# Performance work log

Measured on AMD Instinct MI355X. Metric: run time of the kernel, lower is better.

## Reference

```python
import jax, jax.numpy as jnp
import numpy as np

HEADS = 16


def setup_inputs() -> dict:
    key = jax.random.key(0)
    ks = jax.random.split(key, 7)
    b, n, dim = 4, 1024, 1024
    s = 1.0 / np.sqrt(dim)
    return {
        "x": jax.random.normal(ks[0], (b, n, dim), dtype=jnp.float32),
        "Wq": jax.random.normal(ks[1], (dim, dim), dtype=jnp.float32) * s,
        "bq": jax.random.normal(ks[2], (dim,), dtype=jnp.float32) * 0.01,
        "Wv": jax.random.normal(ks[3], (dim, dim), dtype=jnp.float32) * s,
        "bv": jax.random.normal(ks[4], (dim,), dtype=jnp.float32) * 0.01,
        "Wo": jax.random.normal(ks[5], (dim, dim), dtype=jnp.float32) * s,
        "bo": jax.random.normal(ks[6], (dim,), dtype=jnp.float32) * 0.01,
    }


def reference(x, Wq, bq, Wv, bv, Wo, bo):
    b, n, dim = x.shape
    h = HEADS
    d = dim // h
    scale = d ** -0.5

    # projections (torch Linear: x @ W.T + b), split heads: b n (h d) -> b h n d
    q = (x @ Wq.T + bq).reshape(b, n, h, d).transpose(0, 2, 1, 3)
    v = (x @ Wv.T + bv).reshape(b, n, h, d).transpose(0, 2, 1, 3)

    # pairwise L2 distance scores: ||q_i||^2 - 2 q_i.q_j + ||q_j||^2
    dots = jnp.einsum("bhnd,bhmd->bhnm", q, q)          # [b,h,n,n]
    sq = jnp.sum(q * q, axis=-1)                          # [b,h,n]
    scores = -(sq[..., :, None] - 2.0 * dots + sq[..., None, :]) * scale
    attn = jax.nn.softmax(scores, axis=-1)

    out = jnp.einsum("bhnm,bhmd->bhnd", attn, v)          # [b,h,n,d]
    out = out.transpose(0, 2, 1, 3).reshape(b, n, dim)    # b h n d -> b n (h d)
    return out @ Wo.T + bo
```

## Files before the change

kernel.cpp:

```cpp
#include <hip/hip_runtime.h>
#include <hip/hip_bf16.h>

typedef __hip_bfloat16 bf16;
typedef short short8 __attribute__((ext_vector_type(8)));
typedef float floatx4 __attribute__((ext_vector_type(4)));
typedef unsigned uintx4 __attribute__((ext_vector_type(4)));
typedef unsigned short ushort;

#define MFMA __builtin_amdgcn_mfma_f32_16x16x32_bf16

#define BATCH 4
#define SEQ   1024
#define DIM   1024
#define HEADS 16
#define HD    64
#define RS    72


__device__ __forceinline__ float b2f(ushort u) {
    union { unsigned i; float f; } x; x.i = (unsigned)u << 16; return x.f;
}
__device__ __forceinline__ ushort f2b(float f) {
    union { float f; unsigned i; } x; x.f = f;
    return (ushort)((x.i + 0x7FFFu + ((x.i >> 16) & 1u)) >> 16);
}

__device__ __forceinline__ void nts16(void* p, uint4 v) {
    uintx4 x; x.x = v.x; x.y = v.y; x.z = v.z; x.w = v.w;
    __builtin_nontemporal_store(x, (uintx4*)p);
}
__device__ __forceinline__ void nts16f(void* p, float4 v) {
    floatx4 x; x.x = v.x; x.y = v.y; x.z = v.z; x.w = v.w;
    __builtin_nontemporal_store(x, (floatx4*)p);
}
__device__ __forceinline__ void nts2(ushort* p, ushort v) {
    __builtin_nontemporal_store(v, p);
}

__device__ __forceinline__ void gload16(const ushort* gp, ushort* lp) {
    __builtin_amdgcn_global_load_lds(
        (const __attribute__((address_space(1))) unsigned*)gp,
        (__attribute__((address_space(3))) unsigned*)lp, 16, 0, 0);
}

__device__ __forceinline__ short8 cvt8(uint4 a, uint4 b) {
    const float* f0 = (const float*)&a;
    const float* f1 = (const float*)&b;
    union { __hip_bfloat162 h; unsigned u; } c0, c1, c2, c3;
    float2 p;
    p.x = f0[0]; p.y = f0[1]; c0.h = __float22bfloat162_rn(p);
    p.x = f0[2]; p.y = f0[3]; c1.h = __float22bfloat162_rn(p);
    p.x = f1[0]; p.y = f1[1]; c2.h = __float22bfloat162_rn(p);
    p.x = f1[2]; p.y = f1[3]; c3.h = __float22bfloat162_rn(p);
    short8 s;
    unsigned* su = (unsigned*)&s;
    su[0] = c0.u; su[1] = c1.u; su[2] = c2.u; su[3] = c3.u;
    return s;
}

__global__ __launch_bounds__(256)
void conv_all(const float* __restrict__ x,  const float* __restrict__ Wq,
              const float* __restrict__ Wv, const float* __restrict__ Wo,
              ushort* __restrict__ xb,  ushort* __restrict__ wqb,
              ushort* __restrict__ wvb, ushort* __restrict__ wob, int doWo)
{
    const int b = blockIdx.x;
    const float* src; ushort* dst; size_t off;
    if (b < 2048)      { src = x;  dst = xb;  off = (size_t)b * 256; }
    else if (b < 2560) { src = Wq; dst = wqb; off = (size_t)(b - 2048) * 256; }
    else if (b < 3072) { src = Wv; dst = wvb; off = (size_t)(b - 2560) * 256; }
    else               { if (!doWo) return;
                         src = Wo; dst = wob; off = (size_t)(b - 3072) * 256; }
    off += threadIdx.x;
    const uint4* sv = (const uint4*)src;
    uint4 a = sv[off * 2], c = sv[off * 2 + 1];
    short8 s = cvt8(a, c);
    nts16(dst + off * 8, *(uint4*)&s);
}

template<int OUT, int BDMA>
__global__ __launch_bounds__(256, 3)
void gemm_core(const ushort* __restrict__ Ab,
               const ushort* __restrict__ Wb0, const ushort* __restrict__ Wb1,
               const float* __restrict__ Wf,
               const float* __restrict__ b0, const float* __restrict__ b1,
               ushort* __restrict__ Qd, ushort* __restrict__ Vd,
               float* __restrict__ Fd, float* __restrict__ sqQ)
{
    __shared__ __align__(16) ushort SMEM[2 * 8192 + 2 * 64 * RS];
    const int t = threadIdx.x;
    const int w = t >> 6, lane = t & 63;
    const int lr = lane & 15, quad = lane >> 4;
    const int isV = (!OUT) && (blockIdx.x >= 16);
    const int n0 = (blockIdx.x & 15) * 64;
    const int m0 = blockIdx.y * 128;
    const ushort* __restrict__ Wb   = isV ? Wb1 : Wb0;
    const float*  __restrict__ bias = isV ? b1 : b0;
    const int mw = (w >> 1) * 64, nw = (w & 1) * 32;
    const int ar = t >> 3, ac8 = (t & 7) * 8;
    const int arow = lane >> 3;
    const int acS  = ((lane & 7) ^ arow) * 8;

    ushort* Acur = SMEM;
    ushort* Anxt = SMEM + 8192;
    ushort* Bcur = SMEM + 16384;
    ushort* Bnxt = SMEM + 16384 + (BDMA ? 4096 : 64 * RS);

    uint4 wpre[4];
    #pragma unroll
    for (int i = 0; i < 4; ++i) {
        const int chunk = w * 4 + i;
        gload16(Ab + (size_t)(m0 + chunk * 8 + arow) * DIM + acS,
                Acur + chunk * 512);
    }
    if (BDMA) {
        #pragma unroll
        for (int i = 0; i < 2; ++i) {
            const int c = w * 2 + i;
            gload16(Wb + (size_t)(n0 + c * 8 + arow) * DIM + acS,
                    Bcur + c * 512);
        }
    } else {
        #pragma unroll
        for (int c = 0; c < 2; ++c) {
            const float* wp = Wf + (size_t)(n0 + c * 32 + ar) * DIM + ac8;
            wpre[2 * c]     = *(const uint4*)wp;
            wpre[2 * c + 1] = *(const uint4*)(wp + 4);
        }
        #pragma unroll
        for (int c = 0; c < 2; ++c)
            *(short8*)&Bcur[(c * 32 + ar) * RS + ac8] = cvt8(wpre[2 * c], wpre[2 * c + 1]);
    }
    __syncthreads();

    floatx4 acc[4][2];
    const floatx4 fz = {0.f, 0.f, 0.f, 0.f};
    #pragma unroll
    for (int i = 0; i < 4; ++i)
        #pragma unroll
        for (int j = 0; j < 2; ++j) acc[i][j] = fz;

    for (int kt = 0; kt < 16; ++kt) {
        if (kt < 15) {
            const int k0 = (kt + 1) * 64;
            #pragma unroll
            for (int i = 0; i < 4; ++i) {
                const int chunk = w * 4 + i;
                gload16(Ab + (size_t)(m0 + chunk * 8 + arow) * DIM + k0 + acS,
                        Anxt + chunk * 512);
            }
            if (BDMA) {
                #pragma unroll
                for (int i = 0; i < 2; ++i) {
                    const int c = w * 2 + i;
                    gload16(Wb + (size_t)(n0 + c * 8 + arow) * DIM + k0 + acS,
                            Bnxt + c * 512);
                }
            } else {
                #pragma unroll
                for (int c = 0; c < 2; ++c) {
                    const float* wp = Wf + (size_t)(n0 + c * 32 + ar) * DIM + k0 + ac8;
                    wpre[2 * c]     = *(const uint4*)wp;
                    wpre[2 * c + 1] = *(const uint4*)(wp + 4);
                }
            }
        }
        #pragma unroll
        for (int ks = 0; ks < 2; ++ks) {
            short8 af[4], bfx[2];
            #pragma unroll
            for (int tm = 0; tm < 4; ++tm) {
                const int rowa = mw + tm * 16 + lr;
                const int csw  = (((ks << 2) | quad) ^ (lr & 7)) * 8;
                af[tm] = *(const short8*)&Acur[rowa * 64 + csw];
            }
            #pragma unroll
            for (int tn = 0; tn < 2; ++tn) {
                const int rowb = nw + tn * 16 + lr;
                if (BDMA) {
                    const int csw = (((ks << 2) | quad) ^ (lr & 7)) * 8;
                    bfx[tn] = *(const short8*)&Bcur[rowb * 64 + csw];
                } else {
                    bfx[tn] = *(const short8*)&Bcur[rowb * RS + ks * 32 + quad * 8];
                }
            }
            #pragma unroll
            for (int tm = 0; tm < 4; ++tm)
                #pragma unroll
                for (int tn = 0; tn < 2; ++tn)
                    acc[tm][tn] = MFMA(af[tm], bfx[tn], acc[tm][tn], 0, 0, 0);
        }
        if (!BDMA && kt < 15) {
            #pragma unroll
            for (int c = 0; c < 2; ++c)
                *(short8*)&Bnxt[(c * 32 + ar) * RS + ac8] = cvt8(wpre[2 * c], wpre[2 * c + 1]);
        }
        __syncthreads();
        ushort* tp;
        tp = Acur; Acur = Anxt; Anxt = tp;
        tp = Bcur; Bcur = Bnxt; Bnxt = tp;
    }

    if (OUT) {
        float* TF = (float*)SMEM;
        #pragma unroll
        for (int pass = 0; pass < 2; ++pass) {
            __syncthreads();
            if ((w >> 1) == pass) {
                #pragma unroll
                for (int tn = 0; tn < 2; ++tn) {
                    const float bval = bias[n0 + nw + tn * 16 + lr];
                    #pragma unroll
                    for (int tm = 0; tm < 4; ++tm)
                        #pragma unroll
                        for (int r = 0; r < 4; ++r)
                            TF[(tm * 16 + quad * 4 + r) * 68 + nw + tn * 16 + lr] =
                                acc[tm][tn][r] + bval;
                }
            }
            __syncthreads();
            #pragma unroll
            for (int it = 0; it < 4; ++it) {
                const int cid = it * 256 + t;
                const int row = cid >> 4, c4 = (cid & 15) * 4;
                nts16f(Fd + (size_t)(m0 + pass * 64 + row) * DIM + n0 + c4,
                       *(const float4*)&TF[row * 68 + c4]);
            }
        }
        return;
    }

    const int bb = m0 >> 10, ii0 = m0 & 1023;
    const int head = blockIdx.x & 15;
    const int bh = bb * HEADS + head;
    if (!isV) {
        #pragma unroll
        for (int tn = 0; tn < 2; ++tn) {
            const float bval = bias[n0 + nw + tn * 16 + lr];
            #pragma unroll
            for (int tm = 0; tm < 4; ++tm)
                #pragma unroll
                for (int r = 0; r < 4; ++r)
                    SMEM[(mw + tm * 16 + quad * 4 + r) * 80 + nw + tn * 16 + lr] =
                        f2b(acc[tm][tn][r] + bval);
        }
        __syncthreads();
        {
            const int row = t >> 1, half = t & 1;
            float s = 0.f;
            #pragma unroll
            for (int c = 0; c < 4; ++c) {
                uint4 kk = *(const uint4*)&SMEM[row * 80 + half * 32 + c * 8];
                const ushort* u = (const ushort*)&kk;
                #pragma unroll
                for (int e = 0; e < 8; ++e) { float f = b2f(u[e]); s += f * f; }
            }
            s += __shfl_xor(s, 1);
            if (half == 0) sqQ[(size_t)bh * SEQ + ii0 + row] = s;
        }
        #pragma unroll
        for (int it = 0; it < 4; ++it) {
            const int cid = it * 256 + t;
            const int row = cid >> 3, col8 = (cid & 7) * 8;
            nts16(Qd + ((size_t)bh * SEQ + ii0 + row) * HD + col8,
                  *(const uint4*)&SMEM[row * 80 + col8]);
        }
    } else {
        #pragma unroll
        for (int tn = 0; tn < 2; ++tn) {
            const float bval = bias[n0 + nw + tn * 16 + lr];
            #pragma unroll
            for (int tm = 0; tm < 4; ++tm)
                #pragma unroll
                for (int r = 0; r < 4; ++r)
                    SMEM[(nw + tn * 16 + lr) * 144 + mw + tm * 16 + quad * 4 + r] =
                        f2b(acc[tm][tn][r] + bval);
        }
        __syncthreads();
        #pragma unroll
        for (int it = 0; it < 4; ++it) {
            const int cid = it * 256 + t;
            const int row = cid >> 4, col8 = (cid & 15) * 8;
            nts16(Vd + ((size_t)bh * HD + row) * SEQ + ii0 + col8,
                  *(const uint4*)&SMEM[row * 144 + col8]);
        }
    }
}

__global__ __launch_bounds__(256, 3)
void attn_mfma(const ushort* __restrict__ Q, const ushort* __restrict__ Vt,
               const float* __restrict__ sqG, ushort* __restrict__ O)
{
    __shared__ __align__(16) ushort Ps[128 * RS];
    __shared__ __align__(16) ushort KV[4 * 4096];

    const int t = threadIdx.x;
    const int w = t >> 6, lane = t & 63;
    const int lr = lane & 15, quad = lane >> 4;
    const int id = blockIdx.x;
    const int bh = id & 63;
    const int i0 = (id >> 6) * 128;
    const ushort* __restrict__ Qp = Q  + (size_t)bh * SEQ * HD;
    const ushort* __restrict__ Vp = Vt + (size_t)bh * HD * SEQ;
    const float*  __restrict__ sqB = sqG + (size_t)bh * SEQ;

    const int arow = lane >> 3;
    const int acS  = ((lane & 7) ^ arow) * 8;

    ushort* Kcur = KV;
    ushort* Vcur = KV + 4096;
    ushort* Knxt = KV + 8192;
    ushort* Vnxt = KV + 12288;

    #pragma unroll
    for (int i = 0; i < 2; ++i) {
        const int c = w + i * 4;
        gload16(Qp + (size_t)(c * 8 + arow) * HD + acS, Kcur + c * 512);
        gload16(Vp + (size_t)(c * 8 + arow) * SEQ + acS, Vcur + c * 512);
    }
    #pragma unroll
    for (int it = 0; it < 4; ++it) {
        const int cid = it * 256 + t;
        const int r = cid >> 3, c8 = (cid & 7) * 8;
        *(uint4*)&Ps[r * RS + c8] = *(const uint4*)(Qp + (size_t)(i0 + r) * HD + c8);
    }
    __syncthreads();

    short8 qa[2][2];
    #pragma unroll
    for (int tm = 0; tm < 2; ++tm)
        #pragma unroll
        for (int ks = 0; ks < 2; ++ks)
            qa[tm][ks] = *(const short8*)&Ps[(w * 32 + tm * 16 + lr) * RS + ks * 32 + quad * 8];
    float sqi[2][4];
    #pragma unroll
    for (int tm = 0; tm < 2; ++tm)
        #pragma unroll
        for (int r = 0; r < 4; ++r)
            sqi[tm][r] = sqB[i0 + w * 32 + tm * 16 + quad * 4 + r];

    floatx4 oacc[2][4];
    const floatx4 fz = {0.f, 0.f, 0.f, 0.f};
    float lrow[2][4] = {};
    #pragma unroll
    for (int tm = 0; tm < 2; ++tm)
        #pragma unroll
        for (int td = 0; td < 4; ++td) oacc[tm][td] = fz;

    for (int jt = 0; jt < 16; ++jt) {
        if (jt < 15) {
            const int j0n = (jt + 1) * 64;
            #pragma unroll
            for (int i = 0; i < 2; ++i) {
                const int c = w + i * 4;
                gload16(Qp + (size_t)(j0n + c * 8 + arow) * HD + acS, Knxt + c * 512);
                gload16(Vp + (size_t)(c * 8 + arow) * SEQ + j0n + acS, Vnxt + c * 512);
            }
        }
        float sq4[4];
        #pragma unroll
        for (int tn = 0; tn < 4; ++tn) sq4[tn] = sqB[jt * 64 + tn * 16 + lr];

        short8 kb[4][2];
        #pragma unroll
        for (int tn = 0; tn < 4; ++tn)
            #pragma unroll
            for (int ks = 0; ks < 2; ++ks) {
                const int row = tn * 16 + lr;
                kb[tn][ks] = *(const short8*)&Kcur[row * 64 + ((((ks << 2) | quad)) ^ (lr & 7)) * 8];
            }

        #pragma unroll
        for (int tm = 0; tm < 2; ++tm) {
            floatx4 sacc[4];
            #pragma unroll
            for (int tn = 0; tn < 4; ++tn) {
                floatx4 a = MFMA(qa[tm][0], kb[tn][0], fz, 0, 0, 0);
                sacc[tn]  = MFMA(qa[tm][1], kb[tn][1], a, 0, 0, 0);
            }
            float sc[4][4];
            #pragma unroll
            for (int tn = 0; tn < 4; ++tn) {
                const float msq = -0.125f * sq4[tn];
                #pragma unroll
                for (int r = 0; r < 4; ++r)
                    sc[tn][r] = __expf(0.25f * sacc[tn][r] + msq - 0.125f * sqi[tm][r]);
            }
            #pragma unroll
            for (int r = 0; r < 4; ++r)
                lrow[tm][r] += sc[0][r] + sc[1][r] + sc[2][r] + sc[3][r];
            #pragma unroll
            for (int tp = 0; tp < 2; ++tp)
                #pragma unroll
                for (int r = 0; r < 4; ++r) {
                    float2 fp; fp.x = sc[2 * tp][r]; fp.y = sc[2 * tp + 1][r];
                    union { __hip_bfloat162 h; unsigned u; } cv;
                    cv.h = __float22bfloat162_rn(fp);
                    const int rowb = (w * 32 + tm * 16 + quad * 4 + r) * RS + lr;
                    Ps[rowb + (2 * tp) * 16]     = (ushort)(cv.u & 0xffffu);
                    Ps[rowb + (2 * tp + 1) * 16] = (ushort)(cv.u >> 16);
                }
        }
        short8 pa[2][2], vb[4][2];
        #pragma unroll
        for (int tm = 0; tm < 2; ++tm)
            #pragma unroll
            for (int ks = 0; ks < 2; ++ks)
                pa[tm][ks] = *(const short8*)&Ps[(w * 32 + tm * 16 + lr) * RS + ks * 32 + quad * 8];
        #pragma unroll
        for (int td = 0; td < 4; ++td)
            #pragma unroll
            for (int ks = 0; ks < 2; ++ks) {
                const int row = td * 16 + lr;
                vb[td][ks] = *(const short8*)&Vcur[row * 64 + ((((ks << 2) | quad)) ^ (lr & 7)) * 8];
            }
        #pragma unroll
        for (int tm = 0; tm < 2; ++tm)
            #pragma unroll
            for (int td = 0; td < 4; ++td) {
                oacc[tm][td] = MFMA(pa[tm][0], vb[td][0], oacc[tm][td], 0, 0, 0);
                oacc[tm][td] = MFMA(pa[tm][1], vb[td][1], oacc[tm][td], 0, 0, 0);
            }
        __syncthreads();
        ushort* tp2;
        tp2 = Kcur; Kcur = Knxt; Knxt = tp2;
        tp2 = Vcur; Vcur = Vnxt; Vnxt = tp2;
    }

    const int bb = bh >> 4, head = bh & 15;
    #pragma unroll
    for (int tm = 0; tm < 2; ++tm)
        #pragma unroll
        for (int r = 0; r < 4; ++r) {
            float l = lrow[tm][r];
            l += __shfl_xor(l, 1);
            l += __shfl_xor(l, 2);
            l += __shfl_xor(l, 4);
            l += __shfl_xor(l, 8);
            const float inv = 1.f / l;
            const int row = i0 + w * 32 + tm * 16 + quad * 4 + r;
            #pragma unroll
            for (int td = 0; td < 4; ++td) {
                nts2(O + (size_t)(bb * SEQ + row) * DIM + head * HD + td * 16 + lr,
                     f2b(oacc[tm][td][r] * inv));
            }
        }
}

extern "C" void kernel_launch(void* const* d_in, const int* in_sizes, int n_in,
                              void* d_out, int out_size, void* d_ws, size_t ws_size,
                              hipStream_t stream)
{
    const float* x  = (const float*)d_in[0];
    const float* Wq = (const float*)d_in[1];
    const float* bq = (const float*)d_in[2];
    const float* Wv = (const float*)d_in[3];
    const float* bv = (const float*)d_in[4];
    const float* Wo = (const float*)d_in[5];
    const float* bo = (const float*)d_in[6];

    ushort* Qh = (ushort*)d_ws;
    ushort* Vt = Qh + (size_t)BATCH * HEADS * SEQ * HD;
    ushort* R  = Vt + (size_t)BATCH * HEADS * SEQ * HD;
    const size_t WS3 = (size_t)3 * BATCH * HEADS * SEQ * HD * 2;
    const size_t WOB = (size_t)DIM * DIM * 2;
    const int doWo = ws_size >= WS3 + WOB;
    ushort* Wob = (ushort*)((char*)d_ws + WS3);

    ushort* Wqb = (ushort*)d_out;
    ushort* Wvb = Wqb + (size_t)DIM * DIM;
    float*  sqG = (float*)(Wvb + (size_t)DIM * DIM);

    conv_all<<<3584, 256, 0, stream>>>(x, Wq, Wv, Wo, R, Wqb, Wvb, Wob, doWo);
    gemm_core<0, 1><<<dim3(32, 32), 256, 0, stream>>>(R, Wqb, Wvb, nullptr,
                                                      bq, bv, Qh, Vt, nullptr, sqG);
    attn_mfma<<<512, 256, 0, stream>>>(Qh, Vt, sqG, R);
    if (doWo) {
        gemm_core<1, 1><<<dim3(16, 32), 256, 0, stream>>>(R, Wob, nullptr, nullptr,
                                                          bo, nullptr, nullptr, nullptr,
                                                          (float*)d_out, nullptr);
    } else {
        gemm_core<1, 0><<<dim3(16, 32), 256, 0, stream>>>(R, nullptr, nullptr, Wo,
                                                          bo, nullptr, nullptr, nullptr,
                                                          (float*)d_out, nullptr);
    }
}
```

Before: 171.7 us.

## Fuse Q and V projections into one GEMM sharing the A tile

Replaces the Q/V projection GEMM, which ran 32x32 blocks each computing either Q or V, with a dedicated kernel where each block computes both Q and V for the same 128x64 tile. The x tile is loaded into LDS once and reused for both weight matrices, which halves A-operand global traffic and the number of blocks. In exchange the block uses more LDS and accumulator registers, so launch bounds drop to 2 blocks per CU and the grid shrinks to 512 blocks, which may reduce latency hiding. The output GEMM is split into its own simplified kernel without functional change.

```diff
diff --git a/kernel.cpp b/kernel.cpp
--- a/kernel.cpp
+++ b/kernel.cpp
@@ -78,24 +78,166 @@
     nts16(dst + off * 8, *(uint4*)&s);
 }
 
-template<int OUT, int BDMA>
+__global__ __launch_bounds__(256, 2)
+void gemm_qv(const ushort* __restrict__ Ab,
+             const ushort* __restrict__ Wqb, const ushort* __restrict__ Wvb,
+             const float* __restrict__ bq, const float* __restrict__ bv,
+             ushort* __restrict__ Qd, ushort* __restrict__ Vd,
+             float* __restrict__ sqQ)
+{
+    __shared__ __align__(16) ushort SMEM[32768];
+    const int t = threadIdx.x;
+    const int w = t >> 6, lane = t & 63;
+    const int lr = lane & 15, quad = lane >> 4;
+    const int n0 = blockIdx.x * 64;
+    const int m0 = blockIdx.y * 128;
+    const int mw = (w >> 1) * 64, nw = (w & 1) * 32;
+    const int arow = lane >> 3;
+    const int acS  = ((lane & 7) ^ arow) * 8;
+
+    ushort* Acur = SMEM;
+    ushort* Anxt = SMEM + 8192;
+    ushort* BQc  = SMEM + 16384;
+    ushort* BVc  = SMEM + 20480;
+    ushort* BQn  = SMEM + 24576;
+    ushort* BVn  = SMEM + 28672;
+
+    #pragma unroll
+    for (int i = 0; i < 4; ++i) {
+        const int chunk = w * 4 + i;
+        gload16(Ab + (size_t)(m0 + chunk * 8 + arow) * DIM + acS,
+                Acur + chunk * 512);
+    }
+    #pragma unroll
+    for (int i = 0; i < 2; ++i) {
+        const int c = w * 2 + i;
+        gload16(Wqb + (size_t)(n0 + c * 8 + arow) * DIM + acS, BQc + c * 512);
+        gload16(Wvb + (size_t)(n0 + c * 8 + arow) * DIM + acS, BVc + c * 512);
+    }
+    __syncthreads();
+
+    floatx4 accQ[4][2], accV[4][2];
+    const floatx4 fz = {0.f, 0.f, 0.f, 0.f};
+    #pragma unroll
+    for (int i = 0; i < 4; ++i)
+        #pragma unroll
+        for (int j = 0; j < 2; ++j) { accQ[i][j] = fz; accV[i][j] = fz; }
+
+    for (int kt = 0; kt < 16; ++kt) {
+        if (kt < 15) {
+            const int k0 = (kt + 1) * 64;
+            #pragma unroll
+            for (int i = 0; i < 4; ++i) {
+                const int chunk = w * 4 + i;
+                gload16(Ab + (size_t)(m0 + chunk * 8 + arow) * DIM + k0 + acS,
+                        Anxt + chunk * 512);
+            }
+            #pragma unroll
+            for (int i = 0; i < 2; ++i) {
+                const int c = w * 2 + i;
+                gload16(Wqb + (size_t)(n0 + c * 8 + arow) * DIM + k0 + acS,
+                        BQn + c * 512);
+                gload16(Wvb + (size_t)(n0 + c * 8 + arow) * DIM + k0 + acS,
+                        BVn + c * 512);
+            }
+        }
+        #pragma unroll
+        for (int ks = 0; ks < 2; ++ks) {
+            const int csw = (((ks << 2) | quad) ^ (lr & 7)) * 8;
+            short8 af[4], bqf[2], bvf[2];
+            #pragma unroll
+            for (int tm = 0; tm < 4; ++tm)
+                af[tm] = *(const short8*)&Acur[(mw + tm * 16 + lr) * 64 + csw];
+            #pragma unroll
+            for (int tn = 0; tn < 2; ++tn) {
+                const int rowb = (nw + tn * 16 + lr) * 64 + csw;
+                bqf[tn] = *(const short8*)&BQc[rowb];
+                bvf[tn] = *(const short8*)&BVc[rowb];
+            }
+            #pragma unroll
+            for (int tm = 0; tm < 4; ++tm)
+                #pragma unroll
+                for (int tn = 0; tn < 2; ++tn) {
+                    accQ[tm][tn] = MFMA(af[tm], bqf[tn], accQ[tm][tn], 0, 0, 0);
+                    accV[tm][tn] = MFMA(af[tm], bvf[tn], accV[tm][tn], 0, 0, 0);
+                }
+        }
+        __syncthreads();
+        ushort* tp;
+        tp = Acur; Acur = Anxt; Anxt = tp;
+        tp = BQc;  BQc  = BQn;  BQn  = tp;
+        tp = BVc;  BVc  = BVn;  BVn  = tp;
+    }
+
+    const int bb = m0 >> 10, ii0 = m0 & 1023;
+    const int head = blockIdx.x;
+    const int bh = bb * HEADS + head;
+
+    #pragma unroll
+    for (int tn = 0; tn < 2; ++tn) {
+        const float bval = bq[n0 + nw + tn * 16 + lr];
+        #pragma unroll
+        for (int tm = 0; tm < 4; ++tm)
+            #pragma unroll
+            for (int r = 0; r < 4; ++r)
+                SMEM[(mw + tm * 16 + quad * 4 + r) * 80 + nw + tn * 16 + lr] =
+                    f2b(accQ[tm][tn][r] + bval);
+    }
+    __syncthreads();
+    {
+        const int row = t >> 1, half = t & 1;
+        float s = 0.f;
+        #pragma unroll
+        for (int c = 0; c < 4; ++c) {
+            uint4 kk = *(const uint4*)&SMEM[row * 80 + half * 32 + c * 8];
+            const ushort* u = (const ushort*)&kk;
+            #pragma unroll
+            for (int e = 0; e < 8; ++e) { float f = b2f(u[e]); s += f * f; }
+        }
+        s += __shfl_xor(s, 1);
+        if (half == 0) sqQ[(size_t)bh * SEQ + ii0 + row] = s;
+    }
+    #pragma unroll
+    for (int it = 0; it < 4; ++it) {
+        const int cid = it * 256 + t;
+        const int row = cid >> 3, col8 = (cid & 7) * 8;
+        nts16(Qd + ((size_t)bh * SEQ + ii0 + row) * HD + col8,
+              *(const uint4*)&SMEM[row * 80 + col8]);
+    }
+    __syncthreads();
+
+    #pragma unroll
+    for (int tn = 0; tn < 2; ++tn) {
+        const float bval = bv[n0 + nw + tn * 16 + lr];
+        #pragma unroll
+        for (int tm = 0; tm < 4; ++tm)
+            #pragma unroll
+            for (int r = 0; r < 4; ++r)
+                SMEM[(nw + tn * 16 + lr) * 144 + mw + tm * 16 + quad * 4 + r] =
+                    f2b(accV[tm][tn][r] + bval);
+    }
+    __syncthreads();
+    #pragma unroll
+    for (int it = 0; it < 4; ++it) {
+        const int cid = it * 256 + t;
+        const int row = cid >> 4, col8 = (cid & 15) * 8;
+        nts16(Vd + ((size_t)bh * HD + row) * SEQ + ii0 + col8,
+              *(const uint4*)&SMEM[row * 144 + col8]);
+    }
+}
+
+template<int BDMA>
 __global__ __launch_bounds__(256, 3)
-void gemm_core(const ushort* __restrict__ Ab,
-               const ushort* __restrict__ Wb0, const ushort* __restrict__ Wb1,
-               const float* __restrict__ Wf,
-               const float* __restrict__ b0, const float* __restrict__ b1,
-               ushort* __restrict__ Qd, ushort* __restrict__ Vd,
-               float* __restrict__ Fd, float* __restrict__ sqQ)
+void gemm_out(const ushort* __restrict__ Ab,
+              const ushort* __restrict__ Wb, const float* __restrict__ Wf,
+              const float* __restrict__ bias, float* __restrict__ Fd)
 {
     __shared__ __align__(16) ushort SMEM[2 * 8192 + 2 * 64 * RS];
     const int t = threadIdx.x;
     const int w = t >> 6, lane = t & 63;
     const int lr = lane & 15, quad = lane >> 4;
-    const int isV = (!OUT) && (blockIdx.x >= 16);
-    const int n0 = (blockIdx.x & 15) * 64;
+    const int n0 = blockIdx.x * 64;
     const int m0 = blockIdx.y * 128;
-    const ushort* __restrict__ Wb   = isV ? Wb1 : Wb0;
-    const float*  __restrict__ bias = isV ? b1 : b0;
     const int mw = (w >> 1) * 64, nw = (w & 1) * 32;
     const int ar = t >> 3, ac8 = (t & 7) * 8;
     const int arow = lane >> 3;
@@ -167,22 +309,16 @@
         }
         #pragma unroll
         for (int ks = 0; ks < 2; ++ks) {
+            const int csw = (((ks << 2) | quad) ^ (lr & 7)) * 8;
             short8 af[4], bfx[2];
             #pragma unroll
-            for (int tm = 0; tm < 4; ++tm) {
-                const int rowa = mw + tm * 16 + lr;
-                const int csw  = (((ks << 2) | quad) ^ (lr & 7)) * 8;
-                af[tm] = *(const short8*)&Acur[rowa * 64 + csw];
-            }
+            for (int tm = 0; tm < 4; ++tm)
+                af[tm] = *(const short8*)&Acur[(mw + tm * 16 + lr) * 64 + csw];
             #pragma unroll
             for (int tn = 0; tn < 2; ++tn) {
                 const int rowb = nw + tn * 16 + lr;
-                if (BDMA) {
-                    const int csw = (((ks << 2) | quad) ^ (lr & 7)) * 8;
-                    bfx[tn] = *(const short8*)&Bcur[rowb * 64 + csw];
-                } else {
-                    bfx[tn] = *(const short8*)&Bcur[rowb * RS + ks * 32 + quad * 8];
-                }
+                if (BDMA) bfx[tn] = *(const short8*)&Bcur[rowb * 64 + csw];
+                else      bfx[tn] = *(const short8*)&Bcur[rowb * RS + ks * 32 + quad * 8];
             }
             #pragma unroll
             for (int tm = 0; tm < 4; ++tm)
@@ -201,88 +337,29 @@
         tp = Bcur; Bcur = Bnxt; Bnxt = tp;
     }
 
-    if (OUT) {
-        float* TF = (float*)SMEM;
-        #pragma unroll
-        for (int pass = 0; pass < 2; ++pass) {
-            __syncthreads();
-            if ((w >> 1) == pass) {
-                #pragma unroll
-                for (int tn = 0; tn < 2; ++tn) {
-                    const float bval = bias[n0 + nw + tn * 16 + lr];
+    float* TF = (float*)SMEM;
+    #pragma unroll
+    for (int pass = 0; pass < 2; ++pass) {
+        __syncthreads();
+        if ((w >> 1) == pass) {
+            #pragma unroll
+            for (int tn = 0; tn < 2; ++tn) {
+                const float bval = bias[n0 + nw + tn * 16 + lr];
+                #pragma unroll
+                for (int tm = 0; tm < 4; ++tm)
                     #pragma unroll
-                    for (int tm = 0; tm < 4; ++tm)
-                        #pragma unroll
-                        for (int r = 0; r < 4; ++r)
-                            TF[(tm * 16 + quad * 4 + r) * 68 + nw + tn * 16 + lr] =
-                                acc[tm][tn][r] + bval;
-                }
-            }
-            __syncthreads();
-            #pragma unroll
-            for (int it = 0; it < 4; ++it) {
-                const int cid = it * 256 + t;
-                const int row = cid >> 4, c4 = (cid & 15) * 4;
-                nts16f(Fd + (size_t)(m0 + pass * 64 + row) * DIM + n0 + c4,
-                       *(const float4*)&TF[row * 68 + c4]);
-            }
-        }
-        return;
-    }
-
-    const int bb = m0 >> 10, ii0 = m0 & 1023;
-    const int head = blockIdx.x & 15;
-    const int bh = bb * HEADS + head;
-    if (!isV) {
-        #pragma unroll
-        for (int tn = 0; tn < 2; ++tn) {
-            const float bval = bias[n0 + nw + tn * 16 + lr];
-            #pragma unroll
-            for (int tm = 0; tm < 4; ++tm)
-                #pragma unroll
-                for (int r = 0; r < 4; ++r)
-                    SMEM[(mw + tm * 16 + quad * 4 + r) * 80 + nw + tn * 16 + lr] =
-                        f2b(acc[tm][tn][r] + bval);
+                    for (int r = 0; r < 4; ++r)
+                        TF[(tm * 16 + quad * 4 + r) * 68 + nw + tn * 16 + lr] =
+                            acc[tm][tn][r] + bval;
+            }
         }
         __syncthreads();
-        {
-            const int row = t >> 1, half = t & 1;
-            float s = 0.f;
-            #pragma unroll
-            for (int c = 0; c < 4; ++c) {
-                uint4 kk = *(const uint4*)&SMEM[row * 80 + half * 32 + c * 8];
-                const ushort* u = (const ushort*)&kk;
-                #pragma unroll
-                for (int e = 0; e < 8; ++e) { float f = b2f(u[e]); s += f * f; }
-            }
-            s += __shfl_xor(s, 1);
-            if (half == 0) sqQ[(size_t)bh * SEQ + ii0 + row] = s;
-        }
         #pragma unroll
         for (int it = 0; it < 4; ++it) {
             const int cid = it * 256 + t;
-            const int row = cid >> 3, col8 = (cid & 7) * 8;
-            nts16(Qd + ((size_t)bh * SEQ + ii0 + row) * HD + col8,
-                  *(const uint4*)&SMEM[row * 80 + col8]);
-        }
-    } else {
-        #pragma unroll
-        for (int tn = 0; tn < 2; ++tn) {
-            const float bval = bias[n0 + nw + tn * 16 + lr];
-            #pragma unroll
-            for (int tm = 0; tm < 4; ++tm)
-                #pragma unroll
-                for (int r = 0; r < 4; ++r)
-                    SMEM[(nw + tn * 16 + lr) * 144 + mw + tm * 16 + quad * 4 + r] =
-                        f2b(acc[tm][tn][r] + bval);
-        }
-        __syncthreads();
-        #pragma unroll
-        for (int it = 0; it < 4; ++it) {
-            const int cid = it * 256 + t;
-            const int row = cid >> 4, col8 = (cid & 15) * 8;
-            nts16(Vd + ((size_t)bh * HD + row) * SEQ + ii0 + col8,
-                  *(const uint4*)&SMEM[row * 144 + col8]);
+            const int row = cid >> 4, c4 = (cid & 15) * 4;
+            nts16f(Fd + (size_t)(m0 + pass * 64 + row) * DIM + n0 + c4,
+                   *(const float4*)&TF[row * 68 + c4]);
         }
     }
 }
@@ -472,16 +549,13 @@
     float*  sqG = (float*)(Wvb + (size_t)DIM * DIM);
 
     conv_all<<<3584, 256, 0, stream>>>(x, Wq, Wv, Wo, R, Wqb, Wvb, Wob, doWo);
-    gemm_core<0, 1><<<dim3(32, 32), 256, 0, stream>>>(R, Wqb, Wvb, nullptr,
-                                                      bq, bv, Qh, Vt, nullptr, sqG);
+    gemm_qv<<<dim3(16, 32), 256, 0, stream>>>(R, Wqb, Wvb, bq, bv, Qh, Vt, sqG);
     attn_mfma<<<512, 256, 0, stream>>>(Qh, Vt, sqG, R);
     if (doWo) {
-        gemm_core<1, 1><<<dim3(16, 32), 256, 0, stream>>>(R, Wob, nullptr, nullptr,
-                                                          bo, nullptr, nullptr, nullptr,
-                                                          (float*)d_out, nullptr);
+        gemm_out<1><<<dim3(16, 32), 256, 0, stream>>>(R, Wob, nullptr, bo,
+                                                      (float*)d_out);
     } else {
-        gemm_core<1, 0><<<dim3(16, 32), 256, 0, stream>>>(R, nullptr, nullptr, Wo,
-                                                          bo, nullptr, nullptr, nullptr,
-                                                          (float*)d_out, nullptr);
-    }
-}
+        gemm_out<0><<<dim3(16, 32), 256, 0, stream>>>(R, nullptr, Wo, bo,
+                                                      (float*)d_out);
+    }
+}
```

New measurement: 158.0 us, median of 2. 8.0% less time.
